# Kernel optimization log

Measured on AMD Instinct MI355X. Metric: run time of the kernel, lower is better.

The kernel has to match this reference:

```python
import jax, jax.numpy as jnp
import numpy as np

B, N, U, K = 2, 768, 64, 8
IN = 2 * U + K  # 136
SLOPE = 0.01    # torch LeakyReLU default


def setup_inputs() -> dict:
    key = jax.random.key(0)
    ks = jax.random.split(key, 12)
    seq_embed = jax.random.normal(ks[0], (B, N, U), dtype=jnp.float32)
    vals = jax.random.uniform(ks[1], (N, N, K), dtype=jnp.float32)
    edge = (jax.random.uniform(ks[2], (N, N)) < 0.05) | jnp.eye(N, dtype=bool)
    relational_encoding = vals * edge[:, :, None].astype(jnp.float32)
    s = 0.05
    inp = {"seq_embed": seq_embed, "relational_encoding": relational_encoding}
    # per-hop MLP params: hop k has Linear(IN,IN) then Linear(IN,1); W stored (in,out)
    inp["w1_1"] = jax.random.normal(ks[3], (IN, IN), dtype=jnp.float32) * s
    inp["b1_1"] = jax.random.normal(ks[4], (IN,), dtype=jnp.float32) * s
    inp["w1_2"] = jax.random.normal(ks[5], (IN, 1), dtype=jnp.float32) * s
    inp["b1_2"] = jax.random.normal(ks[6], (1,), dtype=jnp.float32) * s
    inp["w2_1"] = jax.random.normal(ks[7], (IN, IN), dtype=jnp.float32) * s
    inp["b2_1"] = jax.random.normal(ks[8], (IN,), dtype=jnp.float32) * s
    inp["w2_2"] = jax.random.normal(ks[9], (IN, 1), dtype=jnp.float32) * s
    inp["b2_2"] = jax.random.normal(ks[10], (1,), dtype=jnp.float32) * s
    return inp


def _fwd(seq_embed, relational_encoding, hop_params):
    mask = (relational_encoding.sum(-1) > 0).astype(seq_embed.dtype)  # (N,N)
    D = mask.sum(-1)  # (N,) row degree
    rel = relational_encoding[None]  # (1,N,N,K) broadcast over batch
    x = seq_embed
    for layers in hop_params:
        b, n, u = x.shape
        e_i = jnp.broadcast_to(x[:, :, None, :], (b, n, n, u))  # row embed
        e_j = jnp.broadcast_to(x[:, None, :, :], (b, n, n, u))  # col embed
        seq_combined = jnp.concatenate([e_i, e_j], axis=-1)     # (B,N,N,2U)
        combined = jnp.concatenate(
            [seq_combined, jnp.broadcast_to(rel, (b, n, n, rel.shape[-1]))], axis=-1)
        combined = combined * mask[None, :, :, None]
        w = combined
        for (W, bb) in layers:
            w = jax.nn.leaky_relu(w @ W + bb, SLOPE)
        w = w[..., 0] * mask[None]                 # (B,N,N)
        scaled = w / D[None, :, None]              # divide each row i by D[i]
        # weighted neighbor embeds = scaled * e_j, summed over dim 1 (rows)
        x = jnp.einsum('bij,biju->bju', scaled, e_j)
    return x


def reference(seq_embed, relational_encoding, w1_1, b1_1, w1_2, b1_2,
              w2_1, b2_1, w2_2, b2_2):
    hop_params = [[(w1_1, b1_1), (w1_2, b1_2)], [(w2_1, b2_1), (w2_2, b2_2)]]
    return _fwd(seq_embed, relational_encoding, hop_params)
```

## Files before the change

### kernel.cpp

```cpp
#include <hip/hip_runtime.h>

#define NN 768
#define UU 64
#define KK 8
#define INF 136
#define BB 2
#define SLOPE 0.01f
#define RECCAP 61440
#define NP 16
#define PSTRIDE 1552

__device__ __forceinline__ float lrelu(float x) { return x > 0.f ? x : SLOPE * x; }


__device__ __forceinline__ float sum_copies(const float* __restrict__ sp, int bj) {
    float f = 0.f;
#pragma unroll
    for (int p = 0; p < NP; p++) f += sp[p * PSTRIDE + bj];
    return f;
}

__device__ __forceinline__ void pre_rows(int r4base, const float* __restrict__ x,
                                         const float* __restrict__ sc,
                                         const float* __restrict__ W1,
                                         float* __restrict__ A, float* __restrict__ Bv,
                                         float (*xs)[UU], int tid) {
    {
        int rr = tid >> 6, u = tid & 63;
        int bi = r4base + rr;
        float f = sc ? sum_copies(sc, bi) : 1.0f;
        xs[rr][u] = x[(size_t)bi * UU + u] * f;
    }
    __syncthreads();
    int m = tid;
    if (m < INF) {
        float a[4] = {0.f, 0.f, 0.f, 0.f}, bv[4] = {0.f, 0.f, 0.f, 0.f};
        for (int u = 0; u < UU; u++) {
            float wa = W1[u * INF + m];
            float wb = W1[(UU + u) * INF + m];
#pragma unroll
            for (int r = 0; r < 4; r++) {
                a[r]  += xs[r][u] * wa;
                bv[r] += xs[r][u] * wb;
            }
        }
#pragma unroll
        for (int r = 0; r < 4; r++) {
            A [(size_t)(r4base + r) * INF + m] = a[r];
            Bv[(size_t)(r4base + r) * INF + m] = bv[r];
        }
    }
}

__global__ void __launch_bounds__(256) k_fused0(
        const float* __restrict__ rel, const float* __restrict__ seq,
        const float* __restrict__ W1, int* __restrict__ recs,
        float* __restrict__ dinv, int* __restrict__ gcount,
        float* __restrict__ A, float* __restrict__ Bv) {
    __shared__ float xs[4][UU];
    __shared__ int wcnt[4];
    __shared__ int sbase;
    int blk = blockIdx.x;
    int tid = threadIdx.x;

    if (blk >= NN) {
        pre_rows((blk - NN) * 4, seq, nullptr, W1, A, Bv, xs, tid);
        return;
    }

    int i = blk;
    int w = tid >> 6, lane = tid & 63;
    int j0 = w * 192;
    float sums[3];
#pragma unroll
    for (int it = 0; it < 3; it++) {
        int j = j0 + it * 64 + lane;
        const float4* rp = (const float4*)(rel + (size_t)(i * NN + j) * KK);
        float4 a = rp[0], b = rp[1];
        sums[it] = a.x + a.y + a.z + a.w + b.x + b.y + b.z + b.w;
    }
    int cnt = 0;
    int pos[3];
    bool act[3];
#pragma unroll
    for (int it = 0; it < 3; it++) {
        act[it] = sums[it] > 0.f;
        unsigned long long m = __ballot(act[it]);
        pos[it] = cnt + __popcll(m & ((1ull << lane) - 1));
        cnt += __popcll(m);
    }
    if (lane == 0) wcnt[w] = cnt;
    __syncthreads();
    int prefix = 0, total = 0;
#pragma unroll
    for (int ww = 0; ww < 4; ww++) {
        int c = wcnt[ww];
        total += c;
        if (ww < w) prefix += c;
    }
    if (tid == 0) {
        sbase = atomicAdd(gcount, total);
        dinv[i] = 1.0f / (float)total;
    }
    __syncthreads();
    int base = sbase;
#pragma unroll
    for (int it = 0; it < 3; it++) {
        if (act[it]) {
            int rp = base + prefix + pos[it];
            if (rp < RECCAP) recs[rp] = (i << 16) | (j0 + it * 64 + lane);
        }
    }
}

__global__ void __launch_bounds__(256) k_pre(const float* __restrict__ x,
                                             const float* __restrict__ sc,
                                             const float* __restrict__ W1,
                                             float* __restrict__ A, float* __restrict__ Bv) {
    __shared__ float xs[4][UU];
    pre_rows(blockIdx.x * 4, x, sc, W1, A, Bv, xs, threadIdx.x);
}

__global__ void __launch_bounds__(256) k_hop(
        const int* __restrict__ recs, const int* __restrict__ gcount,
        const float* __restrict__ A, const float* __restrict__ Bv,
        const float* __restrict__ rel, const float* __restrict__ W1,
        const float* __restrict__ b1, const float* __restrict__ w2,
        const float* __restrict__ b2, const float* __restrict__ dinv,
        float* __restrict__ sp) {
    int lane = threadIdx.x & 63;
    int wid = (blockIdx.x * blockDim.x + threadIdx.x) >> 6;
    int cnt = *gcount;
    int p = wid * 4;
    if (p >= cnt) return;
    float* s = sp + (wid & (NP - 1)) * PSTRIDE;

    const float* W1R = W1 + 128 * INF;
    float w1r0[8], w1r1[8], w1r2[8];
#pragma unroll
    for (int k = 0; k < 8; k++) {
        w1r0[k] = W1R[k * INF + lane];
        w1r1[k] = W1R[k * INF + 64 + lane];
        w1r2[k] = W1R[k * INF + 128 + (lane & 7)];
    }
    float b10 = b1[lane], b11 = b1[64 + lane], b12 = b1[128 + (lane & 7)];
    float w20 = w2[lane], w21 = w2[64 + lane];
    float w22 = (lane < 8) ? w2[128 + lane] : 0.f;
    float b2v = b2[0];

    int4 q = *(const int4*)(recs + p);
    int rr4[4] = {q.x, q.y, q.z, q.w};

#pragma unroll
    for (int t = 0; t < 4; t++) {
        if (p + t >= cnt) break;
        int rec = rr4[t];
        int i = rec >> 16, j = rec & 0xffff;
        const float* relp = rel + (size_t)(i * NN + j) * KK;
        float4 ra = ((const float4*)relp)[0];
        float4 rb = ((const float4*)relp)[1];
        float di = dinv[i];
        float rv[8] = {ra.x, ra.y, ra.z, ra.w, rb.x, rb.y, rb.z, rb.w};
        float r0 = b10, r1 = b11, r2 = b12;
#pragma unroll
        for (int k = 0; k < 8; k++) {
            r0 += rv[k] * w1r0[k];
            r1 += rv[k] * w1r1[k];
            r2 += rv[k] * w1r2[k];
        }
        float dd[BB];
#pragma unroll
        for (int b = 0; b < BB; b++) {
            const float* Ai = A  + ((size_t)b * NN + i) * INF;
            const float* Bj = Bv + ((size_t)b * NN + j) * INF;
            float dot = lrelu(r0 + Ai[lane]      + Bj[lane])      * w20
                      + lrelu(r1 + Ai[64 + lane] + Bj[64 + lane]) * w21;
            if (lane < 8)
                dot += lrelu(r2 + Ai[128 + lane] + Bj[128 + lane]) * w22;
#pragma unroll
            for (int off = 32; off; off >>= 1) dot += __shfl_xor(dot, off, 64);
            dd[b] = dot;
        }
        if (lane == 0)  atomicAdd(&s[j],      lrelu(dd[0] + b2v) * di);
        if (lane == 32) atomicAdd(&s[NN + j], lrelu(dd[1] + b2v) * di);
    }
}

__global__ void __launch_bounds__(256) k_final(const float4* __restrict__ seq,
                                               const float* __restrict__ s1p,
                                               const float* __restrict__ s2p,
                                               float4* __restrict__ out) {
    int idx = blockIdx.x * blockDim.x + threadIdx.x;
    int bj = idx >> 4;
    float f = sum_copies(s1p, bj) * sum_copies(s2p, bj);
    float4 v = seq[idx];
    v.x *= f; v.y *= f; v.z *= f; v.w *= f;
    out[idx] = v;
}

extern "C" void kernel_launch(void* const* d_in, const int* in_sizes, int n_in,
                              void* d_out, int out_size, void* d_ws, size_t ws_size,
                              hipStream_t stream) {
    const float* seq = (const float*)d_in[0];
    const float* rel = (const float*)d_in[1];
    const float* w1_1 = (const float*)d_in[2];
    const float* b1_1 = (const float*)d_in[3];
    const float* w1_2 = (const float*)d_in[4];
    const float* b1_2 = (const float*)d_in[5];
    const float* w2_1 = (const float*)d_in[6];
    const float* b2_1 = (const float*)d_in[7];
    const float* w2_2 = (const float*)d_in[8];
    const float* b2_2 = (const float*)d_in[9];
    float* out = (float*)d_out;

    char* ws = (char*)d_ws;
    float* s1p    = (float*)(ws + 0);
    float* s2p    = (float*)(ws + 99328);
    int*   gcount = (int*)  (ws + 198656);
    float* dinv   = (float*)(ws + 198912);
    float* A      = (float*)(ws + 202752);
    float* Bv     = (float*)(ws + 1038336);
    int*   recs   = (int*)  (ws + 1873920);

    hipMemsetAsync(ws, 0, 198660, stream);

    k_fused0<<<NN + 384, 256, 0, stream>>>(rel, seq, w1_1, recs, dinv, gcount, A, Bv);

    k_hop<<<RECCAP / 16, 256, 0, stream>>>(recs, gcount, A, Bv, rel, w1_1, b1_1, w1_2, b1_2, dinv, s1p);

    k_pre<<<384, 256, 0, stream>>>(seq, s1p, w2_1, A, Bv);
    k_hop<<<RECCAP / 16, 256, 0, stream>>>(recs, gcount, A, Bv, rel, w2_1, b2_1, w2_2, b2_2, dinv, s2p);

    k_final<<<BB * NN * UU / 4 / 256, 256, 0, stream>>>((const float4*)seq, s1p, s2p, (float4*)out);
}
```

Measured before the change: 143.6 us.

## Fold hop-2 rescale into precomputed projections and use per-row edge slots

```diff
diff --git a/kernel.cpp b/kernel.cpp
--- a/kernel.cpp
+++ b/kernel.cpp
@@ -6,65 +6,58 @@
 #define INF 136
 #define BB 2
 #define SLOPE 0.01f
-#define RECCAP 61440
-#define NP 16
+#define CAP 80
+#define NSLOT (NN*CAP)
+#define NP 4
 #define PSTRIDE 1552
 
 __device__ __forceinline__ float lrelu(float x) { return x > 0.f ? x : SLOPE * x; }
 
 
-__device__ __forceinline__ float sum_copies(const float* __restrict__ sp, int bj) {
-    float f = 0.f;
-#pragma unroll
-    for (int p = 0; p < NP; p++) f += sp[p * PSTRIDE + bj];
-    return f;
-}
-
-__device__ __forceinline__ void pre_rows(int r4base, const float* __restrict__ x,
-                                         const float* __restrict__ sc,
-                                         const float* __restrict__ W1,
+__device__ __forceinline__ void pre_rows(int r4, const float* __restrict__ x,
+                                         const float* __restrict__ W,
                                          float* __restrict__ A, float* __restrict__ Bv,
                                          float (*xs)[UU], int tid) {
-    {
-        int rr = tid >> 6, u = tid & 63;
-        int bi = r4base + rr;
-        float f = sc ? sum_copies(sc, bi) : 1.0f;
-        xs[rr][u] = x[(size_t)bi * UU + u] * f;
-    }
+    { int rr = tid >> 6, u = tid & 63;
+      xs[rr][u] = x[(size_t)(r4 + rr) * UU + u]; }
     __syncthreads();
     int m = tid;
     if (m < INF) {
-        float a[4] = {0.f, 0.f, 0.f, 0.f}, bv[4] = {0.f, 0.f, 0.f, 0.f};
+        float a[4] = {0.f,0.f,0.f,0.f}, bv[4] = {0.f,0.f,0.f,0.f};
         for (int u = 0; u < UU; u++) {
-            float wa = W1[u * INF + m];
-            float wb = W1[(UU + u) * INF + m];
-#pragma unroll
-            for (int r = 0; r < 4; r++) {
-                a[r]  += xs[r][u] * wa;
-                bv[r] += xs[r][u] * wb;
-            }
+            float wa = W[u * INF + m];
+            float wb = W[(UU + u) * INF + m];
+#pragma unroll
+            for (int r = 0; r < 4; r++) { a[r] += xs[r][u] * wa; bv[r] += xs[r][u] * wb; }
         }
 #pragma unroll
         for (int r = 0; r < 4; r++) {
-            A [(size_t)(r4base + r) * INF + m] = a[r];
-            Bv[(size_t)(r4base + r) * INF + m] = bv[r];
-        }
-    }
-}
-
-__global__ void __launch_bounds__(256) k_fused0(
+            A [(size_t)(r4 + r) * INF + m] = a[r];
+            Bv[(size_t)(r4 + r) * INF + m] = bv[r];
+        }
+    }
+}
+
+__global__ void __launch_bounds__(256) k_setup(
         const float* __restrict__ rel, const float* __restrict__ seq,
-        const float* __restrict__ W1, int* __restrict__ recs,
-        float* __restrict__ dinv, int* __restrict__ gcount,
-        float* __restrict__ A, float* __restrict__ Bv) {
+        const float* __restrict__ W1, const float* __restrict__ W2,
+        int* __restrict__ recs, int* __restrict__ rowcnt,
+        float* __restrict__ A, float* __restrict__ Bv,
+        float* __restrict__ P2, float* __restrict__ Q2,
+        float* __restrict__ s1p, float* __restrict__ s2p) {
     __shared__ float xs[4][UU];
     __shared__ int wcnt[4];
-    __shared__ int sbase;
     int blk = blockIdx.x;
     int tid = threadIdx.x;
 
     if (blk >= NN) {
-        pre_rows((blk - NN) * 4, seq, nullptr, W1, A, Bv, xs, tid);
+        int g = blk - NN;
+        bool h2 = g >= 384;
+        if (h2) g -= 384;
+        float* z = h2 ? s2p : s1p;
+        int zi = g * 256 + tid;
+        if (zi < NP * PSTRIDE) z[zi] = 0.f;
+        pre_rows(g * 4, seq, h2 ? W2 : W1, h2 ? P2 : A, h2 ? Q2 : Bv, xs, tid);
         return;
     }
 
@@ -98,91 +91,91 @@
         total += c;
         if (ww < w) prefix += c;
     }
-    if (tid == 0) {
-        sbase = atomicAdd(gcount, total);
-        dinv[i] = 1.0f / (float)total;
-    }
-    __syncthreads();
-    int base = sbase;
+    if (tid == 0) rowcnt[i] = total < CAP ? total : CAP;
 #pragma unroll
     for (int it = 0; it < 3; it++) {
         if (act[it]) {
-            int rp = base + prefix + pos[it];
-            if (rp < RECCAP) recs[rp] = (i << 16) | (j0 + it * 64 + lane);
-        }
-    }
-}
-
-__global__ void __launch_bounds__(256) k_pre(const float* __restrict__ x,
-                                             const float* __restrict__ sc,
-                                             const float* __restrict__ W1,
-                                             float* __restrict__ A, float* __restrict__ Bv) {
-    __shared__ float xs[4][UU];
-    pre_rows(blockIdx.x * 4, x, sc, W1, A, Bv, xs, threadIdx.x);
-}
-
+            int rp = prefix + pos[it];
+            if (rp < CAP) recs[i * CAP + rp] = j0 + it * 64 + lane;
+        }
+    }
+}
+
+template<bool H2>
 __global__ void __launch_bounds__(256) k_hop(
-        const int* __restrict__ recs, const int* __restrict__ gcount,
-        const float* __restrict__ A, const float* __restrict__ Bv,
+        const int* __restrict__ recs, const int* __restrict__ rowcnt,
+        const float* __restrict__ Ar, const float* __restrict__ Br,
         const float* __restrict__ rel, const float* __restrict__ W1,
         const float* __restrict__ b1, const float* __restrict__ w2,
-        const float* __restrict__ b2, const float* __restrict__ dinv,
+        const float* __restrict__ b2, const float* __restrict__ sc,
         float* __restrict__ sp) {
     int lane = threadIdx.x & 63;
     int wid = (blockIdx.x * blockDim.x + threadIdx.x) >> 6;
-    int cnt = *gcount;
-    int p = wid * 4;
-    if (p >= cnt) return;
-    float* s = sp + (wid & (NP - 1)) * PSTRIDE;
+    int i = wid / (CAP / 4);
+    int w0 = (wid - i * (CAP / 4)) * 4;
+    int cnt = rowcnt[i];
+    if (w0 >= cnt) return;
+
+    int hl = lane & 31, b = lane >> 5;
+    int e0 = hl, e1 = 32 + hl, e2 = 64 + hl, e3 = 96 + hl, e4 = 128 + (hl & 7);
 
     const float* W1R = W1 + 128 * INF;
-    float w1r0[8], w1r1[8], w1r2[8];
+    float wr0[8], wr1[8], wr2[8], wr3[8], wr4[8];
 #pragma unroll
     for (int k = 0; k < 8; k++) {
-        w1r0[k] = W1R[k * INF + lane];
-        w1r1[k] = W1R[k * INF + 64 + lane];
-        w1r2[k] = W1R[k * INF + 128 + (lane & 7)];
-    }
-    float b10 = b1[lane], b11 = b1[64 + lane], b12 = b1[128 + (lane & 7)];
-    float w20 = w2[lane], w21 = w2[64 + lane];
-    float w22 = (lane < 8) ? w2[128 + lane] : 0.f;
+        const float* Wk = W1R + k * INF;
+        wr0[k] = Wk[e0]; wr1[k] = Wk[e1]; wr2[k] = Wk[e2]; wr3[k] = Wk[e3]; wr4[k] = Wk[e4];
+    }
+    float bb0 = b1[e0], bb1 = b1[e1], bb2 = b1[e2], bb3 = b1[e3], bb4 = b1[e4];
+    float w20 = w2[e0], w21 = w2[e1], w22 = w2[e2], w23 = w2[e3];
+    float w24 = (hl < 8) ? w2[e4] : 0.f;
     float b2v = b2[0];
-
-    int4 q = *(const int4*)(recs + p);
-    int rr4[4] = {q.x, q.y, q.z, q.w};
+    float di = 1.0f / (float)cnt;
+
+    const float* Ai = Ar + ((size_t)b * NN + i) * INF;
+    float ai0 = Ai[e0], ai1 = Ai[e1], ai2 = Ai[e2], ai3 = Ai[e3], ai4 = Ai[e4];
+    if (H2) {
+        float si = 0.f;
+#pragma unroll
+        for (int p = 0; p < NP; p++) si += sc[p * PSTRIDE + b * NN + i];
+        ai0 *= si; ai1 *= si; ai2 *= si; ai3 *= si; ai4 *= si;
+    }
+
+    float* s = sp + (wid & (NP - 1)) * PSTRIDE + b * NN;
+
+    int4 q = *(const int4*)(recs + i * CAP + w0);
+    int jj[4] = {q.x, q.y, q.z, q.w};
+    int nt = cnt - w0;
 
 #pragma unroll
     for (int t = 0; t < 4; t++) {
-        if (p + t >= cnt) break;
-        int rec = rr4[t];
-        int i = rec >> 16, j = rec & 0xffff;
-        const float* relp = rel + (size_t)(i * NN + j) * KK;
+        if (t >= nt) break;
+        int j = jj[t];
+        const float* relp = rel + ((size_t)i * NN + j) * KK;
         float4 ra = ((const float4*)relp)[0];
         float4 rb = ((const float4*)relp)[1];
-        float di = dinv[i];
         float rv[8] = {ra.x, ra.y, ra.z, ra.w, rb.x, rb.y, rb.z, rb.w};
-        float r0 = b10, r1 = b11, r2 = b12;
+        float r0 = bb0, r1 = bb1, r2 = bb2, r3 = bb3, r4 = bb4;
 #pragma unroll
         for (int k = 0; k < 8; k++) {
-            r0 += rv[k] * w1r0[k];
-            r1 += rv[k] * w1r1[k];
-            r2 += rv[k] * w1r2[k];
-        }
-        float dd[BB];
-#pragma unroll
-        for (int b = 0; b < BB; b++) {
-            const float* Ai = A  + ((size_t)b * NN + i) * INF;
-            const float* Bj = Bv + ((size_t)b * NN + j) * INF;
-            float dot = lrelu(r0 + Ai[lane]      + Bj[lane])      * w20
-                      + lrelu(r1 + Ai[64 + lane] + Bj[64 + lane]) * w21;
-            if (lane < 8)
-                dot += lrelu(r2 + Ai[128 + lane] + Bj[128 + lane]) * w22;
-#pragma unroll
-            for (int off = 32; off; off >>= 1) dot += __shfl_xor(dot, off, 64);
-            dd[b] = dot;
-        }
-        if (lane == 0)  atomicAdd(&s[j],      lrelu(dd[0] + b2v) * di);
-        if (lane == 32) atomicAdd(&s[NN + j], lrelu(dd[1] + b2v) * di);
+            r0 += rv[k] * wr0[k]; r1 += rv[k] * wr1[k]; r2 += rv[k] * wr2[k];
+            r3 += rv[k] * wr3[k]; r4 += rv[k] * wr4[k];
+        }
+        const float* Bj = Br + ((size_t)b * NN + j) * INF;
+        float sj = 1.f;
+        if (H2) {
+            sj = 0.f;
+#pragma unroll
+            for (int p = 0; p < NP; p++) sj += sc[p * PSTRIDE + b * NN + j];
+        }
+        float dot = lrelu(r0 + ai0 + sj * Bj[e0]) * w20
+                  + lrelu(r1 + ai1 + sj * Bj[e1]) * w21
+                  + lrelu(r2 + ai2 + sj * Bj[e2]) * w22
+                  + lrelu(r3 + ai3 + sj * Bj[e3]) * w23
+                  + lrelu(r4 + ai4 + sj * Bj[e4]) * w24;
+#pragma unroll
+        for (int off = 16; off; off >>= 1) dot += __shfl_xor(dot, off, 64);
+        if (hl == 0) atomicAdd(&s[j], lrelu(dot + b2v) * di);
     }
 }
 
@@ -192,7 +185,10 @@
                                                float4* __restrict__ out) {
     int idx = blockIdx.x * blockDim.x + threadIdx.x;
     int bj = idx >> 4;
-    float f = sum_copies(s1p, bj) * sum_copies(s2p, bj);
+    float f1 = 0.f, f2 = 0.f;
+#pragma unroll
+    for (int p = 0; p < NP; p++) { f1 += s1p[p * PSTRIDE + bj]; f2 += s2p[p * PSTRIDE + bj]; }
+    float f = f1 * f2;
     float4 v = seq[idx];
     v.x *= f; v.y *= f; v.z *= f; v.w *= f;
     out[idx] = v;
@@ -201,8 +197,8 @@
 extern "C" void kernel_launch(void* const* d_in, const int* in_sizes, int n_in,
                               void* d_out, int out_size, void* d_ws, size_t ws_size,
                               hipStream_t stream) {
-    const float* seq = (const float*)d_in[0];
-    const float* rel = (const float*)d_in[1];
+    const float* seq  = (const float*)d_in[0];
+    const float* rel  = (const float*)d_in[1];
     const float* w1_1 = (const float*)d_in[2];
     const float* b1_1 = (const float*)d_in[3];
     const float* w1_2 = (const float*)d_in[4];
@@ -214,22 +210,21 @@
     float* out = (float*)d_out;
 
     char* ws = (char*)d_ws;
-    float* s1p    = (float*)(ws + 0);
-    float* s2p    = (float*)(ws + 99328);
-    int*   gcount = (int*)  (ws + 198656);
-    float* dinv   = (float*)(ws + 198912);
-    float* A      = (float*)(ws + 202752);
-    float* Bv     = (float*)(ws + 1038336);
-    int*   recs   = (int*)  (ws + 1873920);
-
-    hipMemsetAsync(ws, 0, 198660, stream);
-
-    k_fused0<<<NN + 384, 256, 0, stream>>>(rel, seq, w1_1, recs, dinv, gcount, A, Bv);
-
-    k_hop<<<RECCAP / 16, 256, 0, stream>>>(recs, gcount, A, Bv, rel, w1_1, b1_1, w1_2, b1_2, dinv, s1p);
-
-    k_pre<<<384, 256, 0, stream>>>(seq, s1p, w2_1, A, Bv);
-    k_hop<<<RECCAP / 16, 256, 0, stream>>>(recs, gcount, A, Bv, rel, w2_1, b2_1, w2_2, b2_2, dinv, s2p);
-
-    k_final<<<BB * NN * UU / 4 / 256, 256, 0, stream>>>((const float4*)seq, s1p, s2p, (float4*)out);
-}
+    float* s1p   = (float*)(ws + 0);
+    float* s2p   = (float*)(ws + 24832);
+    int* rowcnt  = (int*)  (ws + 49664);
+    float* A     = (float*)(ws + 52736);
+    float* Bv    = (float*)(ws + 888320);
+    float* P2    = (float*)(ws + 1723904);
+    float* Q2    = (float*)(ws + 2559488);
+    int* recs    = (int*)  (ws + 3395072);
+
+    k_setup<<<NN + 768, 256, 0, stream>>>(rel, seq, w1_1, w2_1, recs, rowcnt,
+                                          A, Bv, P2, Q2, s1p, s2p);
+    k_hop<false><<<NSLOT / 16, 256, 0, stream>>>(recs, rowcnt, A, Bv, rel,
+                                                 w1_1, b1_1, w1_2, b1_2, nullptr, s1p);
+    k_hop<true><<<NSLOT / 16, 256, 0, stream>>>(recs, rowcnt, P2, Q2, rel,
+                                                w2_1, b2_1, w2_2, b2_2, s1p, s2p);
+    k_final<<<BB * NN * UU / 4 / 256, 256, 0, stream>>>((const float4*)seq, s1p, s2p,
+                                                        (float4*)out);
+}
```

Measured after the change: 128.6 us (median of 2 runs). 1.12x faster.
